# Kernel optimization log

Hardware: AMD Instinct MI355X
Metric: run time of the kernel (lower is better)

Reference implementation:

```python
import jax, jax.numpy as jnp
import numpy as np

RENORM_PERIOD = 256
MAX_NORM = 100.0


def setup_inputs() -> dict:
    key = jax.random.key(0)
    ks = jax.random.split(key, 9)
    B, S, G, D, N = 4, 2048, 8, 128, 64
    return {
        "x_r": jax.random.normal(ks[0], (B, S, G, D), jnp.float32),
        "x_i": jax.random.normal(ks[1], (B, S, G, D), jnp.float32),
        "log_A_mag": jax.random.uniform(ks[2], (G, N), jnp.float32) * 0.5 + 0.5,
        "A_phase": jax.random.normal(ks[3], (G, N), jnp.float32) * 0.1,
        "Bw_r": jax.random.normal(ks[4], (N, D), jnp.float32) / np.sqrt(D),
        "Bw_i": jax.random.normal(ks[5], (N, D), jnp.float32) / np.sqrt(D),
        "Cw_r": jax.random.normal(ks[6], (D, N), jnp.float32) / np.sqrt(N),
        "Cw_i": jax.random.normal(ks[7], (D, N), jnp.float32) / np.sqrt(N),
        "dt_w": jax.random.normal(ks[8], (2, 2 * D), jnp.float32) * 0.02,
        "dt_b": jnp.zeros((2,), jnp.float32),
    }


def reference(x_r, x_i, log_A_mag, A_phase, Bw_r, Bw_i, Cw_r, Cw_i, dt_w, dt_b):
    B, S, G, D = x_r.shape
    N = Bw_r.shape[0]
    # dt: input-dependent step magnitude / phase scale, clamped
    x_cat = jnp.concatenate([x_r, x_i], axis=-1)            # [B,S,G,2D]
    dt = jnp.clip(jnp.exp(jnp.einsum('bsgd,od->bsgo', x_cat, dt_w) + dt_b), 1e-4, 2.0)
    dt_mag = dt[..., 0:1]                                    # [B,S,G,1]
    dt_phase = dt[..., 1:2]
    # A_bar in polar form, |A| = exp(-softplus(log_A_mag)*dt_mag) < 1
    neg_log_A = -jax.nn.softplus(log_A_mag)[None, None]      # [1,1,G,N]
    A_mag = jnp.exp(dt_mag * neg_log_A)                      # [B,S,G,N]
    A_ang = dt_phase * A_phase[None, None]
    A_r = A_mag * jnp.cos(A_ang)
    A_i = A_mag * jnp.sin(A_ang)
    # Bx = (B_proj @ x) * dt_mag, complex linear
    Bx_r = (jnp.einsum('bsgd,nd->bsgn', x_r, Bw_r) - jnp.einsum('bsgd,nd->bsgn', x_i, Bw_i)) * dt_mag
    Bx_i = (jnp.einsum('bsgd,nd->bsgn', x_r, Bw_i) + jnp.einsum('bsgd,nd->bsgn', x_i, Bw_r)) * dt_mag

    def step(carry, inp):
        h_r, h_i = carry
        ar, ai, br, bi, t = inp
        nh_r = ar * h_r - ai * h_i + br
        nh_i = ar * h_i + ai * h_r + bi
        renorm = ((t + 1) % RENORM_PERIOD) == 0
        norm = jnp.sqrt(nh_r * nh_r + nh_i * nh_i + 1e-8)
        scale = jnp.minimum(norm, MAX_NORM) / norm
        nh_r = jnp.where(renorm, nh_r * scale, nh_r)
        nh_i = jnp.where(renorm, nh_i * scale, nh_i)
        return (nh_r, nh_i), (nh_r, nh_i)

    h0 = (jnp.zeros((B, G, N), jnp.float32), jnp.zeros((B, G, N), jnp.float32))
    xs = (jnp.moveaxis(A_r, 1, 0), jnp.moveaxis(A_i, 1, 0),
          jnp.moveaxis(Bx_r, 1, 0), jnp.moveaxis(Bx_i, 1, 0),
          jnp.arange(S))
    _, (all_h_r, all_h_i) = jax.lax.scan(step, h0, xs)       # [S,B,G,N]
    all_h_r = jnp.moveaxis(all_h_r, 0, 1)                    # [B,S,G,N]
    all_h_i = jnp.moveaxis(all_h_i, 0, 1)
    # y = C_proj(h), complex linear N -> D
    y_r = jnp.einsum('bsgn,dn->bsgd', all_h_r, Cw_r) - jnp.einsum('bsgn,dn->bsgd', all_h_i, Cw_i)
    y_i = jnp.einsum('bsgn,dn->bsgd', all_h_r, Cw_i) + jnp.einsum('bsgn,dn->bsgd', all_h_i, Cw_r)
    return jnp.stack([y_r, y_i], axis=0)                     # [2,B,S,G,D]
```

## Files before the change

kernel.cpp:

```cpp
#include <hip/hip_runtime.h>
#include <math.h>

#define B_ 4
#define S_ 2048
#define G_ 8
#define D_ 128
#define N_ 64
#define ROWS (B_*S_*G_)
#define CH 64
#define CLEN 32
#define NCHAIN (B_*G_*N_)
#define YOFF (ROWS*D_)

typedef short bf16x8 __attribute__((ext_vector_type(8)));
typedef float f32x4  __attribute__((ext_vector_type(4)));
#define MFMA16(a,b,c) __builtin_amdgcn_mfma_f32_16x16x32_bf16(a,b,c,0,0,0)

__device__ __forceinline__ unsigned short bf16_rtne(float f) {
    unsigned u = __float_as_uint(f);
    unsigned r = (u + 0x7FFFu + ((u >> 16) & 1u)) >> 16;
    return (unsigned short)r;
}
__device__ __forceinline__ void split_bf16(float f, unsigned short &hi, unsigned short &lo) {
    hi = bf16_rtne(f);
    float hif = __uint_as_float(((unsigned)hi) << 16);
    lo = bf16_rtne(f - hif);
}
__device__ __forceinline__ void split4(float4 v, uint2 &hi2, uint2 &lo2) {
    unsigned short h0,h1,h2,h3,l0,l1,l2,l3;
    split_bf16(v.x,h0,l0); split_bf16(v.y,h1,l1);
    split_bf16(v.z,h2,l2); split_bf16(v.w,h3,l3);
    hi2 = make_uint2((unsigned)h0 | ((unsigned)h1<<16), (unsigned)h2 | ((unsigned)h3<<16));
    lo2 = make_uint2((unsigned)l0 | ((unsigned)l1<<16), (unsigned)l2 | ((unsigned)l3<<16));
}
__device__ __forceinline__ float dot4(float4 a, float4 b) {
    return fmaf(a.x,b.x, fmaf(a.y,b.y, fmaf(a.z,b.z, a.w*b.w)));
}

__global__ __launch_bounds__(256) void k_prep(
    const float* __restrict__ bwr, const float* __restrict__ bwi,
    const float* __restrict__ cwr, const float* __restrict__ cwi,
    unsigned short* __restrict__ wbhi, unsigned short* __restrict__ wblo,
    unsigned short* __restrict__ wchi)
{
    int tid = blockIdx.x * 256 + threadIdx.x;
    if (tid < 4096) {
        int f = tid;
        int lane = f & 63, ks = (f >> 6) & 7, nt = (f >> 9) & 1, w = f >> 10;
        int l15 = lane & 15, quad = lane >> 4;
        int n = w * 32 + nt * 16 + l15;
        int k0 = ks * 32 + quad * 8;
        const float* src; float sgn = 1.f;
        if (n < 64) {
            if (k0 < 128) src = bwr + n * 128 + k0;
            else        { src = bwi + n * 128 + (k0 - 128); sgn = -1.f; }
        } else {
            if (k0 < 128) src = bwi + (n - 64) * 128 + k0;
            else          src = bwr + (n - 64) * 128 + (k0 - 128);
        }
        float4 v0 = *(const float4*)src;
        float4 v1 = *(const float4*)(src + 4);
        float vv[8] = {v0.x,v0.y,v0.z,v0.w,v1.x,v1.y,v1.z,v1.w};
        unsigned short h[8], l[8];
        #pragma unroll
        for (int j = 0; j < 8; j++) split_bf16(vv[j] * sgn, h[j], l[j]);
        #pragma unroll
        for (int j = 0; j < 8; j++) { wbhi[f*8+j] = h[j]; wblo[f*8+j] = l[j]; }
    } else {
        int f = tid - 4096;
        int lane = f & 63, ks = (f >> 6) & 3, nt = (f >> 8) & 3, w = f >> 10;
        int l15 = lane & 15, quad = lane >> 4;
        int n = w * 64 + nt * 16 + l15;
        int d = (n < 128) ? n : (n - 128);
        int k0 = ks * 32 + quad * 8;
        const float* src; float sgn = 1.f;
        if (n < 128) {
            if (k0 < 64) src = cwr + d * 64 + k0;
            else       { src = cwi + d * 64 + (k0 - 64); sgn = -1.f; }
        } else {
            if (k0 < 64) src = cwi + d * 64 + k0;
            else         src = cwr + d * 64 + (k0 - 64);
        }
        float4 v0 = *(const float4*)src;
        float4 v1 = *(const float4*)(src + 4);
        float vv[8] = {v0.x,v0.y,v0.z,v0.w,v1.x,v1.y,v1.z,v1.w};
        unsigned short h[8], l[8];
        #pragma unroll
        for (int j = 0; j < 8; j++) split_bf16(vv[j] * sgn, h[j], l[j]);
        #pragma unroll
        for (int j = 0; j < 8; j++) wchi[f*8+j] = h[j];
    }
}

#define LDK1 280
__global__ __launch_bounds__(256, 2) void k_g1(
    const float* __restrict__ xr, const float* __restrict__ xi,
    const float* __restrict__ dtw, const float* __restrict__ dtb,
    const unsigned short* __restrict__ wbhi, const unsigned short* __restrict__ wblo,
    float* __restrict__ bxr, float* __restrict__ bxi,
    float* __restrict__ dt_mag, float* __restrict__ dt_ph)
{
    __shared__ __align__(16) unsigned short Ahi[32 * LDK1];
    __shared__ __align__(16) unsigned short Alo[32 * LDK1];
    __shared__ float dms[32];
    const int t = threadIdx.x;
    const int lane = t & 63, w = t >> 6;
    const int l15 = lane & 15, quad = lane >> 4;

    bf16x8 wh[2][8], wl[2][8];
    #pragma unroll
    for (int nt = 0; nt < 2; nt++)
        #pragma unroll
        for (int ks = 0; ks < 8; ks++) {
            int idx = ((w * 2 + nt) * 8 + ks) * 64 + lane;
            wh[nt][ks] = ((const bf16x8*)wbhi)[idx];
            wl[nt][ks] = ((const bf16x8*)wblo)[idx];
        }

    const int kq = t & 31, k4 = kq * 4;
    float4 w0r = *(const float4*)(dtw + k4);
    float4 w0i = *(const float4*)(dtw + 128 + k4);
    float4 w1r = *(const float4*)(dtw + 256 + k4);
    float4 w1i = *(const float4*)(dtw + 384 + k4);
    float b0 = dtb[0], b1 = dtb[1];

    for (int it = 0; it < 4; it++) {
        const int R0 = (blockIdx.x * 4 + it) * 32;
        const float4* gxr = (const float4*)(xr + R0 * 128);
        const float4* gxi = (const float4*)(xi + R0 * 128);
        float pm[4], pp[4];
        #pragma unroll
        for (int i = 0; i < 4; i++) {
            int f = t + 256 * i;
            int m = f >> 5;
            float4 a = gxr[f];
            float4 b = gxi[f];
            uint2 h2, l2;
            split4(a, h2, l2);
            *(uint2*)&Ahi[m * LDK1 + k4] = h2;
            *(uint2*)&Alo[m * LDK1 + k4] = l2;
            split4(b, h2, l2);
            *(uint2*)&Ahi[m * LDK1 + 128 + k4] = h2;
            *(uint2*)&Alo[m * LDK1 + 128 + k4] = l2;
            pm[i] = dot4(a, w0r) + dot4(b, w0i);
            pp[i] = dot4(a, w1r) + dot4(b, w1i);
        }
        #pragma unroll
        for (int i = 0; i < 4; i++) {
            float vm = pm[i], vp = pp[i];
            #pragma unroll
            for (int msk = 16; msk >= 1; msk >>= 1) {
                vm += __shfl_xor(vm, msk);
                vp += __shfl_xor(vp, msk);
            }
            if ((t & 31) == 0) {
                int m = (t >> 5) + 8 * i;
                float dm = fminf(fmaxf(__expf(vm + b0), 1e-4f), 2.0f);
                float dp = fminf(fmaxf(__expf(vp + b1), 1e-4f), 2.0f);
                dms[m] = dm;
                dt_mag[R0 + m] = dm; dt_ph[R0 + m] = dp;
            }
        }
        __syncthreads();

        f32x4 acc[2][2];
        #pragma unroll
        for (int a = 0; a < 2; a++)
            #pragma unroll
            for (int b = 0; b < 2; b++)
                acc[a][b] = (f32x4){0.f, 0.f, 0.f, 0.f};
        #pragma unroll
        for (int ms = 0; ms < 2; ms++) {
            int arow = (ms * 16 + l15) * LDK1 + quad * 8;
            #pragma unroll
            for (int ks = 0; ks < 8; ks++) {
                bf16x8 ah = *(const bf16x8*)&Ahi[arow + ks * 32];
                bf16x8 al = *(const bf16x8*)&Alo[arow + ks * 32];
                #pragma unroll
                for (int nt = 0; nt < 2; nt++) {
                    acc[ms][nt] = MFMA16(al, wh[nt][ks], acc[ms][nt]);
                    acc[ms][nt] = MFMA16(ah, wl[nt][ks], acc[ms][nt]);
                    acc[ms][nt] = MFMA16(ah, wh[nt][ks], acc[ms][nt]);
                }
            }
        }
        #pragma unroll
        for (int ms = 0; ms < 2; ms++)
            #pragma unroll
            for (int nt = 0; nt < 2; nt++) {
                int n = w * 32 + nt * 16 + l15;
                float* dst = (n < 64) ? bxr : bxi;
                int nn = n & 63;
                #pragma unroll
                for (int r = 0; r < 4; r++) {
                    int m = ms * 16 + quad * 4 + r;
                    dst[(R0 + m) * 64 + nn] = acc[ms][nt][r] * dms[m];
                }
            }
        __syncthreads();
    }
}

__global__ __launch_bounds__(256) void k_scanA(const float* __restrict__ dt_mag,
    const float* __restrict__ dt_ph, const float* __restrict__ logAm,
    const float* __restrict__ Aph, const float* __restrict__ bxr,
    const float* __restrict__ bxi, float4* __restrict__ trans)
{
    int tid = blockIdx.x * 256 + threadIdx.x;
    int n  = tid & 63;
    int c  = (tid >> 6) & 63;
    int bg = tid >> 12;
    int g = bg & 7, b = bg >> 3;
    float nla = -logf(1.0f + __expf(logAm[g * N_ + n]));
    float aph = Aph[g * N_ + n];
    float Ar = 1.f, Ai = 0.f, Br = 0.f, Bi = 0.f;
    int s0 = c * CLEN;
    #pragma unroll 4
    for (int tt = 0; tt < CLEN; tt++) {
        int row = (b * S_ + s0 + tt) * G_ + g;
        float dm = dt_mag[row], dp = dt_ph[row];
        float am  = __expf(dm * nla);
        float ang = dp * aph;
        float cr = am * __cosf(ang), ci = am * __sinf(ang);
        float vr = bxr[row * N_ + n], vi = bxi[row * N_ + n];
        float nAr = cr * Ar - ci * Ai;
        float nAi = cr * Ai + ci * Ar;
        float nBr = cr * Br - ci * Bi + vr;
        float nBi = cr * Bi + ci * Br + vi;
        Ar = nAr; Ai = nAi; Br = nBr; Bi = nBi;
    }
    trans[tid] = make_float4(Ar, Ai, Br, Bi);
}

__global__ __launch_bounds__(256) void k_scanB(const float4* __restrict__ trans,
    float2* __restrict__ hstart)
{
    int tid = blockIdx.x * 256 + threadIdx.x;
    int n = tid & 63;
    int bg = tid >> 6;
    float hr = 0.f, hi = 0.f;
    for (int c = 0; c < CH; c++) {
        int idx = (bg * CH + c) * 64 + n;
        hstart[idx] = make_float2(hr, hi);
        float4 T = trans[idx];
        float nr = T.x * hr - T.y * hi + T.z;
        float ni = T.x * hi + T.y * hr + T.w;
        if ((c & 7) == 7) {
            float nrm = sqrtf(nr * nr + ni * ni + 1e-8f);
            float scale = fminf(nrm, 100.0f) / nrm;
            nr *= scale; ni *= scale;
        }
        hr = nr; hi = ni;
    }
}

#define LDK2 152
__global__ __launch_bounds__(256, 2) void k_sg2(
    const float* __restrict__ bxr, const float* __restrict__ bxi,
    const float* __restrict__ dt_mag, const float* __restrict__ dt_ph,
    const float* __restrict__ logAm, const float* __restrict__ Aph,
    const float2* __restrict__ hstart,
    const unsigned short* __restrict__ wchi,
    float* __restrict__ out)
{
    __shared__ __align__(16) unsigned short Ahi[128 * LDK2];
    __shared__ __align__(16) unsigned short Alo[128 * LDK2];
    const int t = threadIdx.x;
    const int lane = t & 63, w = t >> 6;
    const int l15 = lane & 15, quad = lane >> 4;
    const int bg = blockIdx.x >> 4, cq = blockIdx.x & 15;
    const int g = bg & 7, b = bg >> 3;

    bf16x8 wc[4][4];
    #pragma unroll
    for (int nt = 0; nt < 4; nt++)
        #pragma unroll
        for (int ks = 0; ks < 4; ks++)
            wc[nt][ks] = ((const bf16x8*)wchi)[((w * 4 + nt) * 4 + ks) * 64 + lane];

    {
        const int n = lane;
        const int c = cq * 4 + w;
        float nla = -logf(1.0f + __expf(logAm[g * N_ + n]));
        float aph = Aph[g * N_ + n];
        float2 h0 = hstart[(bg * CH + c) * 64 + n];
        float hr = h0.x, hi = h0.y;
        const bool rn = ((c & 7) == 7);
        const int rowbase = (b * S_ + c * CLEN) * G_ + g;
        #pragma unroll 8
        for (int tt = 0; tt < CLEN; tt++) {
            int row = rowbase + tt * G_;
            float dm = dt_mag[row], dp = dt_ph[row];
            float am  = __expf(dm * nla);
            float ang = dp * aph;
            float cr = am * __cosf(ang), ci = am * __sinf(ang);
            float vr = bxr[row * N_ + n], vi = bxi[row * N_ + n];
            float nr = cr * hr - ci * hi + vr;
            float ni = cr * hi + ci * hr + vi;
            if (rn && tt == CLEN - 1) {
                float nrm = sqrtf(nr * nr + ni * ni + 1e-8f);
                float scale = fminf(nrm, 100.0f) / nrm;
                nr *= scale; ni *= scale;
            }
            hr = nr; hi = ni;
            int m = w * 32 + tt;
            unsigned short hh, hl;
            split_bf16(hr, hh, hl);
            Ahi[m * LDK2 + n] = hh;  Alo[m * LDK2 + n] = hl;
            split_bf16(hi, hh, hl);
            Ahi[m * LDK2 + 64 + n] = hh;  Alo[m * LDK2 + 64 + n] = hl;
        }
    }
    __syncthreads();

    #pragma unroll
    for (int mh = 0; mh < 2; mh++) {
        f32x4 acc[4][4];
        #pragma unroll
        for (int a = 0; a < 4; a++)
            #pragma unroll
            for (int bq = 0; bq < 4; bq++)
                acc[a][bq] = (f32x4){0.f, 0.f, 0.f, 0.f};
        #pragma unroll
        for (int ms = 0; ms < 4; ms++) {
            int arow = (mh * 64 + ms * 16 + l15) * LDK2 + quad * 8;
            #pragma unroll
            for (int ks = 0; ks < 4; ks++) {
                bf16x8 ah = *(const bf16x8*)&Ahi[arow + ks * 32];
                bf16x8 al = *(const bf16x8*)&Alo[arow + ks * 32];
                #pragma unroll
                for (int nt = 0; nt < 4; nt++) {
                    acc[ms][nt] = MFMA16(al, wc[nt][ks], acc[ms][nt]);
                    acc[ms][nt] = MFMA16(ah, wc[nt][ks], acc[ms][nt]);
                }
            }
        }
        #pragma unroll
        for (int ms = 0; ms < 4; ms++)
            #pragma unroll
            for (int nt = 0; nt < 4; nt++) {
                int nn = w * 64 + nt * 16 + l15;
                float* dst = (nn < 128) ? (out + nn) : (out + YOFF + (nn - 128));
                #pragma unroll
                for (int r = 0; r < 4; r++) {
                    int m_local = mh * 64 + ms * 16 + quad * 4 + r;
                    int cc = m_local >> 5, tt2 = m_local & 31;
                    int srow = (b * S_ + (cq * 4 + cc) * CLEN + tt2) * G_ + g;
                    dst[srow * 128] = acc[ms][nt][r];
                }
            }
    }
}

extern "C" void kernel_launch(void* const* d_in, const int* in_sizes, int n_in,
                              void* d_out, int out_size, void* d_ws, size_t ws_size,
                              hipStream_t stream) {
    (void)in_sizes; (void)n_in; (void)out_size; (void)ws_size;
    const float* xr    = (const float*)d_in[0];
    const float* xi    = (const float*)d_in[1];
    const float* logAm = (const float*)d_in[2];
    const float* Aph   = (const float*)d_in[3];
    const float* bwr   = (const float*)d_in[4];
    const float* bwi   = (const float*)d_in[5];
    const float* cwr   = (const float*)d_in[6];
    const float* cwi   = (const float*)d_in[7];
    const float* dtw   = (const float*)d_in[8];
    const float* dtb   = (const float*)d_in[9];
    float* out = (float*)d_out;
    float* ws  = (float*)d_ws;

    float*  dt_mag = ws;
    float*  dt_ph  = ws + 65536;
    float*  bxr    = ws + 131072;
    float*  bxi    = bxr + 4194304;
    float4* trans  = (float4*)(ws + 8519680);
    float2* hstart = (float2*)(ws + 9043968);
    unsigned short* wbhi = (unsigned short*)(ws + 9306112);
    unsigned short* wblo = wbhi + 32768;
    unsigned short* wchi = wblo + 32768;

    hipLaunchKernelGGL(k_prep,  dim3(32), dim3(256), 0, stream,
                       bwr, bwi, cwr, cwi, wbhi, wblo, wchi);
    hipLaunchKernelGGL(k_g1,    dim3(ROWS / 128), dim3(256), 0, stream,
                       xr, xi, dtw, dtb, wbhi, wblo, bxr, bxi, dt_mag, dt_ph);
    hipLaunchKernelGGL(k_scanA, dim3((NCHAIN * CH) / 256), dim3(256), 0, stream,
                       dt_mag, dt_ph, logAm, Aph, bxr, bxi, trans);
    hipLaunchKernelGGL(k_scanB, dim3(NCHAIN / 256), dim3(256), 0, stream,
                       trans, hstart);
    hipLaunchKernelGGL(k_sg2,   dim3((B_ * G_) * 16), dim3(256), 0, stream,
                       bxr, bxi, dt_mag, dt_ph, logAm, Aph, hstart, wchi, out);
}
```

Baseline: 174.1 us.

## Fuse chunk-local scan into B-projection GEMM and parallelize cross-chunk scan

The GEMM kernel now assigns each block a (batch, group) pair and four consecutive 32-step chunks. It computes each chunk's scan transfer (A, B composition) from the just-produced Bx values staged in shared memory, so the separate scanA kernel and its reread of Bx from global memory are gone. The sequential 64-step cross-chunk scan is replaced by a two-level scan that spreads eight sub-chunks across lanes and combines them with shuffles, applying renormalization at the same chunk boundaries as before. The cost is strided x loads, extra barriers and only two waves doing the serial in-block scan while the others idle.

```diff
diff --git a/kernel.cpp b/kernel.cpp
--- a/kernel.cpp
+++ b/kernel.cpp
@@ -96,16 +96,22 @@
 __global__ __launch_bounds__(256, 2) void k_g1(
     const float* __restrict__ xr, const float* __restrict__ xi,
     const float* __restrict__ dtw, const float* __restrict__ dtb,
+    const float* __restrict__ logAm, const float* __restrict__ Aph,
     const unsigned short* __restrict__ wbhi, const unsigned short* __restrict__ wblo,
     float* __restrict__ bxr, float* __restrict__ bxi,
-    float* __restrict__ dt_mag, float* __restrict__ dt_ph)
+    float* __restrict__ dt_mag, float* __restrict__ dt_ph,
+    float4* __restrict__ trans)
 {
     __shared__ __align__(16) unsigned short Ahi[32 * LDK1];
     __shared__ __align__(16) unsigned short Alo[32 * LDK1];
-    __shared__ float dms[32];
+    __shared__ float dms[32], dps[32];
+    __shared__ float4 comb[64];
+    float* bxs = (float*)Ahi;
     const int t = threadIdx.x;
     const int lane = t & 63, w = t >> 6;
     const int l15 = lane & 15, quad = lane >> 4;
+    const int bg = blockIdx.x >> 4, cq = blockIdx.x & 15;
+    const int g = bg & 7, b = bg >> 3;
 
     bf16x8 wh[2][8], wl[2][8];
     #pragma unroll
@@ -123,27 +129,31 @@
     float4 w1r = *(const float4*)(dtw + 256 + k4);
     float4 w1i = *(const float4*)(dtw + 384 + k4);
     float b0 = dtb[0], b1 = dtb[1];
+    float nla = -logf(1.0f + __expf(logAm[g * N_ + lane]));
+    float aph = Aph[g * N_ + lane];
 
     for (int it = 0; it < 4; it++) {
-        const int R0 = (blockIdx.x * 4 + it) * 32;
-        const float4* gxr = (const float4*)(xr + R0 * 128);
-        const float4* gxi = (const float4*)(xi + R0 * 128);
+        __syncthreads();
+        const int c  = cq * 4 + it;
+        const int s0 = c * CLEN;
+        const float* xrb = xr + ((size_t)(b * S_ + s0) * G_ + g) * 128;
+        const float* xib = xi + ((size_t)(b * S_ + s0) * G_ + g) * 128;
         float pm[4], pp[4];
         #pragma unroll
         for (int i = 0; i < 4; i++) {
             int f = t + 256 * i;
-            int m = f >> 5;
-            float4 a = gxr[f];
-            float4 b = gxi[f];
+            int m = f >> 5, kk = f & 31;
+            float4 a  = ((const float4*)(xrb + m * 1024))[kk];
+            float4 bb = ((const float4*)(xib + m * 1024))[kk];
             uint2 h2, l2;
             split4(a, h2, l2);
-            *(uint2*)&Ahi[m * LDK1 + k4] = h2;
-            *(uint2*)&Alo[m * LDK1 + k4] = l2;
-            split4(b, h2, l2);
-            *(uint2*)&Ahi[m * LDK1 + 128 + k4] = h2;
-            *(uint2*)&Alo[m * LDK1 + 128 + k4] = l2;
-            pm[i] = dot4(a, w0r) + dot4(b, w0i);
-            pp[i] = dot4(a, w1r) + dot4(b, w1i);
+            *(uint2*)&Ahi[m * LDK1 + kk * 4] = h2;
+            *(uint2*)&Alo[m * LDK1 + kk * 4] = l2;
+            split4(bb, h2, l2);
+            *(uint2*)&Ahi[m * LDK1 + 128 + kk * 4] = h2;
+            *(uint2*)&Alo[m * LDK1 + 128 + kk * 4] = l2;
+            pm[i] = dot4(a, w0r) + dot4(bb, w0i);
+            pp[i] = dot4(a, w1r) + dot4(bb, w1i);
         }
         #pragma unroll
         for (int i = 0; i < 4; i++) {
@@ -157,8 +167,9 @@
                 int m = (t >> 5) + 8 * i;
                 float dm = fminf(fmaxf(__expf(vm + b0), 1e-4f), 2.0f);
                 float dp = fminf(fmaxf(__expf(vp + b1), 1e-4f), 2.0f);
-                dms[m] = dm;
-                dt_mag[R0 + m] = dm; dt_ph[R0 + m] = dp;
+                dms[m] = dm; dps[m] = dp;
+                int row = (b * S_ + s0 + m) * G_ + g;
+                dt_mag[row] = dm; dt_ph[row] = dp;
             }
         }
         __syncthreads();
@@ -167,8 +178,8 @@
         #pragma unroll
         for (int a = 0; a < 2; a++)
             #pragma unroll
-            for (int b = 0; b < 2; b++)
-                acc[a][b] = (f32x4){0.f, 0.f, 0.f, 0.f};
+            for (int bq = 0; bq < 2; bq++)
+                acc[a][bq] = (f32x4){0.f, 0.f, 0.f, 0.f};
         #pragma unroll
         for (int ms = 0; ms < 2; ms++) {
             int arow = (ms * 16 + l15) * LDK1 + quad * 8;
@@ -184,73 +195,96 @@
                 }
             }
         }
+        __syncthreads();
+
         #pragma unroll
         for (int ms = 0; ms < 2; ms++)
             #pragma unroll
             for (int nt = 0; nt < 2; nt++) {
                 int n = w * 32 + nt * 16 + l15;
-                float* dst = (n < 64) ? bxr : bxi;
+                float* dstg = (n < 64) ? bxr : bxi;
                 int nn = n & 63;
                 #pragma unroll
                 for (int r = 0; r < 4; r++) {
                     int m = ms * 16 + quad * 4 + r;
-                    dst[(R0 + m) * 64 + nn] = acc[ms][nt][r] * dms[m];
+                    float v = acc[ms][nt][r] * dms[m];
+                    dstg[((b * S_ + s0 + m) * G_ + g) * 64 + nn] = v;
+                    bxs[m * 132 + n] = v;
                 }
             }
         __syncthreads();
-    }
-}
-
-__global__ __launch_bounds__(256) void k_scanA(const float* __restrict__ dt_mag,
-    const float* __restrict__ dt_ph, const float* __restrict__ logAm,
-    const float* __restrict__ Aph, const float* __restrict__ bxr,
-    const float* __restrict__ bxi, float4* __restrict__ trans)
-{
-    int tid = blockIdx.x * 256 + threadIdx.x;
-    int n  = tid & 63;
-    int c  = (tid >> 6) & 63;
-    int bg = tid >> 12;
-    int g = bg & 7, b = bg >> 3;
-    float nla = -logf(1.0f + __expf(logAm[g * N_ + n]));
-    float aph = Aph[g * N_ + n];
-    float Ar = 1.f, Ai = 0.f, Br = 0.f, Bi = 0.f;
-    int s0 = c * CLEN;
-    #pragma unroll 4
-    for (int tt = 0; tt < CLEN; tt++) {
-        int row = (b * S_ + s0 + tt) * G_ + g;
-        float dm = dt_mag[row], dp = dt_ph[row];
-        float am  = __expf(dm * nla);
-        float ang = dp * aph;
-        float cr = am * __cosf(ang), ci = am * __sinf(ang);
-        float vr = bxr[row * N_ + n], vi = bxi[row * N_ + n];
-        float nAr = cr * Ar - ci * Ai;
-        float nAi = cr * Ai + ci * Ar;
-        float nBr = cr * Br - ci * Bi + vr;
-        float nBi = cr * Bi + ci * Br + vi;
-        Ar = nAr; Ai = nAi; Br = nBr; Bi = nBi;
-    }
-    trans[tid] = make_float4(Ar, Ai, Br, Bi);
-}
-
-__global__ __launch_bounds__(256) void k_scanB(const float4* __restrict__ trans,
+
+        float Ar = 1.f, Ai = 0.f, Br = 0.f, Bi = 0.f;
+        if (w < 2) {
+            int base = w * 16;
+            #pragma unroll
+            for (int tt = 0; tt < 16; tt++) {
+                int m = base + tt;
+                float dm = dms[m], dp = dps[m];
+                float am  = __expf(dm * nla);
+                float ang = dp * aph;
+                float cr = am * __cosf(ang), ci = am * __sinf(ang);
+                float vr = bxs[m * 132 + lane], vi = bxs[m * 132 + 64 + lane];
+                float nAr = cr * Ar - ci * Ai;
+                float nAi = cr * Ai + ci * Ar;
+                float nBr = cr * Br - ci * Bi + vr;
+                float nBi = cr * Bi + ci * Br + vi;
+                Ar = nAr; Ai = nAi; Br = nBr; Bi = nBi;
+            }
+            if (w == 0) comb[lane] = make_float4(Ar, Ai, Br, Bi);
+        }
+        __syncthreads();
+        if (w == 1) {
+            float4 c0 = comb[lane];
+            float fAr = Ar * c0.x - Ai * c0.y;
+            float fAi = Ar * c0.y + Ai * c0.x;
+            float fBr = Ar * c0.z - Ai * c0.w + Br;
+            float fBi = Ar * c0.w + Ai * c0.z + Bi;
+            trans[(bg * CH + c) * 64 + lane] = make_float4(fAr, fAi, fBr, fBi);
+        }
+    }
+}
+
+__global__ __launch_bounds__(256) void k_scanB2(const float4* __restrict__ trans,
     float2* __restrict__ hstart)
 {
-    int tid = blockIdx.x * 256 + threadIdx.x;
-    int n = tid & 63;
-    int bg = tid >> 6;
-    float hr = 0.f, hi = 0.f;
-    for (int c = 0; c < CH; c++) {
-        int idx = (bg * CH + c) * 64 + n;
-        hstart[idx] = make_float2(hr, hi);
-        float4 T = trans[idx];
-        float nr = T.x * hr - T.y * hi + T.z;
-        float ni = T.x * hi + T.y * hr + T.w;
-        if ((c & 7) == 7) {
-            float nrm = sqrtf(nr * nr + ni * ni + 1e-8f);
-            float scale = fminf(nrm, 100.0f) / nrm;
-            nr *= scale; ni *= scale;
-        }
-        hr = nr; hi = ni;
+    int w = threadIdx.x >> 6, lane = threadIdx.x & 63;
+    int W = blockIdx.x * 4 + w;
+    int bg = W >> 3;
+    int n  = ((W & 7) << 3) + (lane & 7);
+    int j  = lane >> 3;
+    float pAr[8], pAi[8], pBr[8], pBi[8];
+    float Ar = 1.f, Ai = 0.f, Br = 0.f, Bi = 0.f;
+    const float4* tp = trans + (bg * CH + j * 8) * 64 + n;
+    #pragma unroll
+    for (int k = 0; k < 8; k++) {
+        pAr[k] = Ar; pAi[k] = Ai; pBr[k] = Br; pBi[k] = Bi;
+        float4 T = tp[k * 64];
+        float nAr = T.x * Ar - T.y * Ai;
+        float nAi = T.x * Ai + T.y * Ar;
+        float nBr = T.x * Br - T.y * Bi + T.z;
+        float nBi = T.x * Bi + T.y * Br + T.w;
+        Ar = nAr; Ai = nAi; Br = nBr; Bi = nBi;
+    }
+    float hr = 0.f, hi = 0.f, mhr = 0.f, mhi = 0.f;
+    #pragma unroll
+    for (int j2 = 0; j2 < 8; j2++) {
+        if (j2 == j) { mhr = hr; mhi = hi; }
+        int src = j2 * 8 + (lane & 7);
+        float sAr = __shfl(Ar, src), sAi = __shfl(Ai, src);
+        float sBr = __shfl(Br, src), sBi = __shfl(Bi, src);
+        float nr = sAr * hr - sAi * hi + sBr;
+        float ni = sAr * hi + sAi * hr + sBi;
+        float nrm = sqrtf(nr * nr + ni * ni + 1e-8f);
+        float sc = fminf(nrm, 100.f) / nrm;
+        hr = nr * sc; hi = ni * sc;
+    }
+    float2* hp = hstart + (bg * CH + j * 8) * 64 + n;
+    #pragma unroll
+    for (int k = 0; k < 8; k++) {
+        float hsr = pAr[k] * mhr - pAi[k] * mhi + pBr[k];
+        float hsi = pAr[k] * mhi + pAi[k] * mhr + pBi[k];
+        hp[k * 64] = make_float2(hsr, hsi);
     }
 }
 
@@ -379,14 +413,13 @@
     unsigned short* wblo = wbhi + 32768;
     unsigned short* wchi = wblo + 32768;
 
-    hipLaunchKernelGGL(k_prep,  dim3(32), dim3(256), 0, stream,
+    hipLaunchKernelGGL(k_prep,   dim3(32), dim3(256), 0, stream,
                        bwr, bwi, cwr, cwi, wbhi, wblo, wchi);
-    hipLaunchKernelGGL(k_g1,    dim3(ROWS / 128), dim3(256), 0, stream,
-                       xr, xi, dtw, dtb, wbhi, wblo, bxr, bxi, dt_mag, dt_ph);
-    hipLaunchKernelGGL(k_scanA, dim3((NCHAIN * CH) / 256), dim3(256), 0, stream,
-                       dt_mag, dt_ph, logAm, Aph, bxr, bxi, trans);
-    hipLaunchKernelGGL(k_scanB, dim3(NCHAIN / 256), dim3(256), 0, stream,
+    hipLaunchKernelGGL(k_g1,     dim3((B_ * G_) * 16), dim3(256), 0, stream,
+                       xr, xi, dtw, dtb, logAm, Aph, wbhi, wblo,
+                       bxr, bxi, dt_mag, dt_ph, trans);
+    hipLaunchKernelGGL(k_scanB2, dim3(64), dim3(256), 0, stream,
                        trans, hstart);
-    hipLaunchKernelGGL(k_sg2,   dim3((B_ * G_) * 16), dim3(256), 0, stream,
+    hipLaunchKernelGGL(k_sg2,    dim3((B_ * G_) * 16), dim3(256), 0, stream,
                        bxr, bxi, dt_mag, dt_ph, logAm, Aph, hstart, wchi, out);
 }
```

Result: faster. 163.7 us (-5.9%).
